# Optimization experiments

Hardware: AMD Instinct MI355X
Metric: run time of the kernel (lower is better)

Reference implementation:

```python
import jax, jax.numpy as jnp
import numpy as np

D_MODEL = 1024
NUM_HEADS = 16
HEAD_DIM = D_MODEL // NUM_HEADS


def setup_inputs() -> dict:
    key = jax.random.key(0)
    ks = jax.random.split(key, 11)
    B, S = 4, 2048
    s = 1.0 / np.sqrt(D_MODEL)
    inp = {
        "query": jax.random.normal(ks[0], (B, S, D_MODEL), jnp.float32),
        "key": jax.random.normal(ks[1], (B, S, D_MODEL), jnp.float32),
        "value": jax.random.normal(ks[2], (B, S, D_MODEL), jnp.float32),
        "Wq": jax.random.normal(ks[3], (D_MODEL, D_MODEL), jnp.float32) * s,
        "bq": jnp.zeros((D_MODEL,), jnp.float32),
        "Wk": jax.random.normal(ks[4], (D_MODEL, D_MODEL), jnp.float32) * s,
        "bk": jnp.zeros((D_MODEL,), jnp.float32),
        "Wv": jax.random.normal(ks[5], (D_MODEL, D_MODEL), jnp.float32) * s,
        "bv": jnp.zeros((D_MODEL,), jnp.float32),
        "Wo": jax.random.normal(ks[6], (D_MODEL, D_MODEL), jnp.float32) * s,
        "bo": jnp.zeros((D_MODEL,), jnp.float32),
    }
    return inp


def reference(query, key, value, Wq, bq, Wk, bk, Wv, bv, Wo, bo):
    B, S, _ = query.shape
    def proj(x, W, b):  # [B,S,D] -> [B,H,S,hd]
        y = jnp.einsum("bsd,ed->bse", x, W) + b
        return y.reshape(B, -1, NUM_HEADS, HEAD_DIM).transpose(0, 2, 1, 3)
    q = proj(query, Wq, bq)
    k = proj(key, Wk, bk)
    v = proj(value, Wv, bv)
    scores = jnp.einsum("bhqd,bhkd->bhqk", q, k) / np.sqrt(HEAD_DIM).astype(jnp.float32)
    attn = jax.nn.softmax(scores, axis=-1)
    out = jnp.einsum("bhqk,bhkd->bhqd", attn, v)
    out = out.transpose(0, 2, 1, 3).reshape(B, -1, D_MODEL)
    return jnp.einsum("bsd,ed->bse", out, Wo) + bo
```

## Files before the change

kernel.cpp:

```cpp
#include <hip/hip_runtime.h>
#include <math.h>

#define DM    1024
#define NH    16
#define HD    64
#define SEQ   2048
#define BATCH 4
#define TOKENS (BATCH * SEQ)

typedef _Float16 half2v __attribute__((ext_vector_type(2)));
typedef __fp16   fp16x2 __attribute__((ext_vector_type(2)));
typedef _Float16 half4  __attribute__((ext_vector_type(4)));
typedef _Float16 half8  __attribute__((ext_vector_type(8)));
typedef float    f32x4  __attribute__((ext_vector_type(4)));
typedef float    f32x16 __attribute__((ext_vector_type(16)));
typedef unsigned int u32x2 __attribute__((ext_vector_type(2)));
typedef unsigned int u32x4 __attribute__((ext_vector_type(4)));

typedef const __attribute__((address_space(1))) void* gas_p;
typedef __attribute__((address_space(3))) void*       las_p;

__device__ __forceinline__ void gload_lds16(const void* g, void* l) {
    __builtin_amdgcn_global_load_lds((gas_p)g, (las_p)l, 16, 0, 0);
}

__device__ __forceinline__ unsigned pack2u(float a, float b) {
    fp16x2 r = __builtin_amdgcn_cvt_pkrtz(a, b);
    return __builtin_bit_cast(unsigned, r);
}

#define MFMA16(a, b, c) __builtin_amdgcn_mfma_f32_16x16x32_f16((a), (b), (c), 0, 0, 0)
#define MFMA32(a, b, c) __builtin_amdgcn_mfma_f32_32x32x16_f16((a), (b), (c), 0, 0, 0)

__global__ __launch_bounds__(256) void cvt_all(
    const float* __restrict__ q, const float* __restrict__ k,
    const float* __restrict__ v, const float* __restrict__ wq,
    const float* __restrict__ wk, const float* __restrict__ wv,
    const float* __restrict__ wo, _Float16* __restrict__ dst)
{
    const size_t TD = (size_t)TOKENS * DM, WD = (size_t)DM * DM;
    const size_t i = ((size_t)blockIdx.x * 256 + threadIdx.x) * 4;
    const float* s; size_t off;
    if      (i <     TD)          { s = q;  off = i; }
    else if (i < 2 * TD)          { s = k;  off = i - TD; }
    else if (i < 3 * TD)          { s = v;  off = i - 2 * TD; }
    else if (i < 3 * TD + WD)     { s = wq; off = i - 3 * TD; }
    else if (i < 3 * TD + 2 * WD) { s = wk; off = i - 3 * TD - WD; }
    else if (i < 3 * TD + 3 * WD) { s = wv; off = i - 3 * TD - 2 * WD; }
    else                          { s = wo; off = i - 3 * TD - 3 * WD; }
    const float4 x = *(const float4*)(s + off);
    half4 h = { (_Float16)x.x, (_Float16)x.y, (_Float16)x.z, (_Float16)x.w };
    *(half4*)(dst + i) = h;
}

__global__ __launch_bounds__(256) void qkv_gemm(
    const _Float16* __restrict__ Abase, const _Float16* __restrict__ Wbase,
    const float* __restrict__ bq, const float* __restrict__ bk,
    const float* __restrict__ bv, _Float16* __restrict__ Cbase, float qscale)
{
    __shared__ __align__(16) _Float16 As[128 * 32];
    __shared__ __align__(16) _Float16 Ws[128 * 32];

    const int z = blockIdx.z;
    const size_t TD = (size_t)TOKENS * DM, WD = (size_t)DM * DM;
    const _Float16* A = Abase + (size_t)z * TD;
    const _Float16* W = Wbase + (size_t)z * WD;
    const float* bias = (z == 0) ? bq : (z == 1) ? bk : bv;
    _Float16* C = Cbase + (size_t)z * TD;
    const float scale = (z == 0) ? qscale : 1.0f;

    const int t = threadIdx.x;
    const int w = t >> 6, l = t & 63;
    const int tx = l & 15, quad = l >> 4;
    const int m0 = blockIdx.x * 128, n0 = blockIdx.y * 128;
    const int wm = (w & 1) * 64, wn = (w >> 1) * 64;
    const int srow = t >> 2, schk = t & 3;

    const _Float16* Ag = A + (size_t)m0 * DM;
    const _Float16* Wg = W + (size_t)n0 * DM;

    f32x4 acc[4][4] = {};

    for (int k0 = 0; k0 < DM; k0 += 32) {
        __syncthreads();
        #pragma unroll
        for (int i = 0; i < 2; ++i) {
            gload_lds16(Ag + (size_t)(i * 64 + srow) * DM + k0 + schk * 8,
                        As + (size_t)(i * 256 + (t & ~63)) * 8);
            gload_lds16(Wg + (size_t)(i * 64 + srow) * DM + k0 + schk * 8,
                        Ws + (size_t)(i * 256 + (t & ~63)) * 8);
        }
        __syncthreads();

        half8 af[4], bf[4];
        #pragma unroll
        for (int mt = 0; mt < 4; ++mt)
            af[mt] = *(const half8*)(As + (wm + mt * 16 + tx) * 32 + quad * 8);
        #pragma unroll
        for (int nt = 0; nt < 4; ++nt)
            bf[nt] = *(const half8*)(Ws + (wn + nt * 16 + tx) * 32 + quad * 8);
        #pragma unroll
        for (int mt = 0; mt < 4; ++mt)
            #pragma unroll
            for (int nt = 0; nt < 4; ++nt)
                acc[mt][nt] = MFMA16(af[mt], bf[nt], acc[mt][nt]);
    }

    float bsv[4];
    #pragma unroll
    for (int nt = 0; nt < 4; ++nt) bsv[nt] = bias[n0 + wn + nt * 16 + tx];

    #pragma unroll
    for (int mt = 0; mt < 4; ++mt) {
        #pragma unroll
        for (int nt = 0; nt < 4; ++nt) {
            const int n = n0 + wn + nt * 16 + tx;
            const int mr0 = m0 + wm + mt * 16 + quad * 4;
            const int h = n >> 6, d = n & 63;
            if (z < 2) {
                #pragma unroll
                for (int r = 0; r < 4; ++r) {
                    const int m = mr0 + r;
                    const int b = m >> 11, s = m & (SEQ - 1);
                    const float vv = (acc[mt][nt][r] + bsv[nt]) * scale;
                    C[(((size_t)b * NH + h) * SEQ + s) * HD + d] = (_Float16)vv;
                }
            } else {
                const int b = mr0 >> 11, s0 = mr0 & (SEQ - 1);
                half4 hv = { (_Float16)(acc[mt][nt][0] + bsv[nt]),
                             (_Float16)(acc[mt][nt][1] + bsv[nt]),
                             (_Float16)(acc[mt][nt][2] + bsv[nt]),
                             (_Float16)(acc[mt][nt][3] + bsv[nt]) };
                *(half4*)(C + (((size_t)b * NH + h) * HD + d) * SEQ + s0) = hv;
            }
        }
    }
}

__global__ __launch_bounds__(256) void out_gemm(
    const _Float16* __restrict__ A, const _Float16* __restrict__ W,
    const float* __restrict__ bias, float* __restrict__ C)
{
    __shared__ __align__(16) _Float16 As[128 * 32];
    __shared__ __align__(16) _Float16 Ws[128 * 32];

    const int t = threadIdx.x;
    const int w = t >> 6, l = t & 63;
    const int tx = l & 15, quad = l >> 4;
    const int m0 = blockIdx.x * 128, n0 = blockIdx.y * 128;
    const int wm = (w & 1) * 64, wn = (w >> 1) * 64;
    const int srow = t >> 2, schk = t & 3;

    const _Float16* Ag = A + (size_t)m0 * DM;
    const _Float16* Wg = W + (size_t)n0 * DM;

    f32x4 acc[4][4] = {};

    for (int k0 = 0; k0 < DM; k0 += 32) {
        __syncthreads();
        #pragma unroll
        for (int i = 0; i < 2; ++i) {
            gload_lds16(Ag + (size_t)(i * 64 + srow) * DM + k0 + schk * 8,
                        As + (size_t)(i * 256 + (t & ~63)) * 8);
            gload_lds16(Wg + (size_t)(i * 64 + srow) * DM + k0 + schk * 8,
                        Ws + (size_t)(i * 256 + (t & ~63)) * 8);
        }
        __syncthreads();

        half8 af[4], bf[4];
        #pragma unroll
        for (int mt = 0; mt < 4; ++mt)
            af[mt] = *(const half8*)(As + (wm + mt * 16 + tx) * 32 + quad * 8);
        #pragma unroll
        for (int nt = 0; nt < 4; ++nt)
            bf[nt] = *(const half8*)(Ws + (wn + nt * 16 + tx) * 32 + quad * 8);
        #pragma unroll
        for (int mt = 0; mt < 4; ++mt)
            #pragma unroll
            for (int nt = 0; nt < 4; ++nt)
                acc[mt][nt] = MFMA16(af[mt], bf[nt], acc[mt][nt]);
    }

    float bsv[4];
    #pragma unroll
    for (int nt = 0; nt < 4; ++nt) bsv[nt] = bias[n0 + wn + nt * 16 + tx];

    #pragma unroll
    for (int mt = 0; mt < 4; ++mt)
        #pragma unroll
        for (int nt = 0; nt < 4; ++nt) {
            const int n = n0 + wn + nt * 16 + tx;
            const int mr0 = m0 + wm + mt * 16 + quad * 4;
            #pragma unroll
            for (int r = 0; r < 4; ++r)
                C[(size_t)(mr0 + r) * DM + n] = acc[mt][nt][r] + bsv[nt];
        }
}

__global__ __launch_bounds__(64, 2) void flash16(
    const _Float16* __restrict__ Q, const _Float16* __restrict__ K,
    const _Float16* __restrict__ Vt, _Float16* __restrict__ AO)
{
    __shared__ __align__(16) float Ob[64 * 69];
    __shared__ float lw[64];

    const int l = threadIdx.x;
    const int lid = l & 31, hl = l >> 5;

    const int bid = blockIdx.x;
    const int xcd = bid & 7, loc = bid >> 3;
    const int bh = xcd * 8 + (loc >> 5);
    const int q0 = (loc & 31) * 64;
    const int b = bh >> 4, h = bh & 15;

    const _Float16* Qg = Q + ((size_t)bh * SEQ + q0) * HD;
    const _Float16* Kg = K + (size_t)bh * SEQ * HD;
    const _Float16* Vg = Vt + (size_t)bh * HD * SEQ;

    half8 Qf[2][4];
    #pragma unroll
    for (int qq = 0; qq < 2; ++qq)
        #pragma unroll
        for (int ks = 0; ks < 4; ++ks)
            Qf[qq][ks] = *(const half8*)(Qg + (size_t)(qq * 32 + lid) * HD + ks * 16 + hl * 8);

    f32x16 Oa[2][2] = {};
    float l2[2] = {0.f, 0.f};
    const half2v one2 = { (_Float16)1.0f, (_Float16)1.0f };

    for (int it = 0; it < SEQ / 64; ++it) {
        const int kb = it * 64;

        half8 kf[2][4];
        #pragma unroll
        for (int kt = 0; kt < 2; ++kt)
            #pragma unroll
            for (int ks = 0; ks < 4; ++ks)
                kf[kt][ks] = *(const half8*)(Kg + (size_t)(kb + kt * 32 + lid) * HD +
                                             ks * 16 + hl * 8);

        half8 vf[4][2];
        #pragma unroll
        for (int kstep = 0; kstep < 4; ++kstep)
            #pragma unroll
            for (int dt = 0; dt < 2; ++dt)
                vf[kstep][dt] = *(const half8*)(Vg + (size_t)(dt * 32 + lid) * SEQ +
                                                kb + kstep * 16 + hl * 8);

        half8 pa[2][4];
        #pragma unroll
        for (int qq = 0; qq < 2; ++qq) {
            f32x16 sacc[2];
            __builtin_amdgcn_s_setprio(1);
            #pragma unroll
            for (int kt = 0; kt < 2; ++kt) {
                f32x16 s = {};
                #pragma unroll
                for (int ks = 0; ks < 4; ++ks)
                    s = MFMA32(kf[kt][ks], Qf[qq][ks], s);
                sacc[kt] = s;
            }
            __builtin_amdgcn_s_setprio(0);

            unsigned cf[2][4][2];
            #pragma unroll
            for (int kt = 0; kt < 2; ++kt)
                #pragma unroll
                for (int g = 0; g < 4; ++g) {
                    const float p0 = __builtin_amdgcn_exp2f(sacc[kt][g * 4 + 0]);
                    const float p1 = __builtin_amdgcn_exp2f(sacc[kt][g * 4 + 1]);
                    const float p2 = __builtin_amdgcn_exp2f(sacc[kt][g * 4 + 2]);
                    const float p3 = __builtin_amdgcn_exp2f(sacc[kt][g * 4 + 3]);
                    const unsigned ca = pack2u(p0, p1);
                    const unsigned cb = pack2u(p2, p3);
                    l2[qq] = __builtin_amdgcn_fdot2(__builtin_bit_cast(half2v, ca), one2, l2[qq], false);
                    l2[qq] = __builtin_amdgcn_fdot2(__builtin_bit_cast(half2v, cb), one2, l2[qq], false);
                    cf[kt][g][0] = ca;
                    cf[kt][g][1] = cb;
                }

            #pragma unroll
            for (int kstep = 0; kstep < 4; ++kstep) {
                const int kt = kstep >> 1, g0 = (kstep & 1) * 2;
                const u32x2 r0 = __builtin_amdgcn_permlane32_swap(
                    cf[kt][g0][0], cf[kt][g0 + 1][0], false, false);
                const u32x2 r1 = __builtin_amdgcn_permlane32_swap(
                    cf[kt][g0][1], cf[kt][g0 + 1][1], false, false);
                const u32x4 pw = { r0[0], r1[0], r0[1], r1[1] };
                pa[qq][kstep] = __builtin_bit_cast(half8, pw);
            }
        }

        __builtin_amdgcn_s_setprio(1);
        #pragma unroll
        for (int kstep = 0; kstep < 4; ++kstep)
            #pragma unroll
            for (int qq = 0; qq < 2; ++qq)
                #pragma unroll
                for (int dt = 0; dt < 2; ++dt)
                    Oa[qq][dt] = MFMA32(pa[qq][kstep], vf[kstep][dt], Oa[qq][dt]);
        __builtin_amdgcn_s_setprio(0);
    }

    #pragma unroll
    for (int qq = 0; qq < 2; ++qq)
        l2[qq] += __shfl_xor(l2[qq], 32, 64);
    if (l < 32) {
        lw[l] = l2[0];
        lw[32 + l] = l2[1];
    }

    #pragma unroll
    for (int qq = 0; qq < 2; ++qq)
        #pragma unroll
        for (int dt = 0; dt < 2; ++dt)
            #pragma unroll
            for (int g = 0; g < 4; ++g)
                #pragma unroll
                for (int r = 0; r < 4; ++r)
                    Ob[(qq * 32 + g * 8 + hl * 4 + r) * 69 + dt * 32 + lid] =
                        Oa[qq][dt][g * 4 + r];
    __syncthreads();

    {
        const float inv = 1.0f / lw[l];
        _Float16* dst = AO + ((size_t)b * SEQ + q0 + l) * DM + h * HD;
        #pragma unroll
        for (int j = 0; j < 64; j += 8) {
            const f32x4 o0 = *(const f32x4*)(Ob + l * 69 + j);
            const f32x4 o1 = *(const f32x4*)(Ob + l * 69 + j + 4);
            half8 hv = { (_Float16)(o0[0] * inv), (_Float16)(o0[1] * inv),
                         (_Float16)(o0[2] * inv), (_Float16)(o0[3] * inv),
                         (_Float16)(o1[0] * inv), (_Float16)(o1[1] * inv),
                         (_Float16)(o1[2] * inv), (_Float16)(o1[3] * inv) };
            *(half8*)(dst + j) = hv;
        }
    }
}

extern "C" void kernel_launch(void* const* d_in, const int* in_sizes, int n_in,
                              void* d_out, int out_size, void* d_ws, size_t ws_size,
                              hipStream_t stream)
{
    const float* q  = (const float*)d_in[0];
    const float* k  = (const float*)d_in[1];
    const float* v  = (const float*)d_in[2];
    const float* Wq = (const float*)d_in[3];
    const float* bq = (const float*)d_in[4];
    const float* Wk = (const float*)d_in[5];
    const float* bk = (const float*)d_in[6];
    const float* Wv = (const float*)d_in[7];
    const float* bv = (const float*)d_in[8];
    const float* Wo = (const float*)d_in[9];
    const float* bo = (const float*)d_in[10];
    float* out = (float*)d_out;

    const size_t TD = (size_t)TOKENS * DM;
    const size_t WD = (size_t)DM * DM;
    _Float16* ws = (_Float16*)d_ws;
    _Float16* cvtbase = ws;
    _Float16* q16  = ws;
    _Float16* wq16 = ws + 3 * TD;
    _Float16* wo16 = wq16 + 3 * WD;
    _Float16* Qw   = ws + 3 * TD + 4 * WD;
    _Float16* Kw   = Qw + TD;
    _Float16* Vtw  = Kw + TD;
    _Float16* AOw  = Vtw + TD;

    const int gC = (int)((3 * TD + 4 * WD) / 4 / 256);
    cvt_all<<<gC, 256, 0, stream>>>(q, k, v, Wq, Wk, Wv, Wo, cvtbase);

    const float qscale = 0.18033688011112042f;
    qkv_gemm<<<dim3(TOKENS / 128, DM / 128, 3), 256, 0, stream>>>(
        q16, wq16, bq, bk, bv, Qw, qscale);

    flash16<<<dim3((SEQ / 64) * BATCH * NH), 64, 0, stream>>>(Qw, Kw, Vtw, AOw);

    out_gemm<<<dim3(TOKENS / 128, DM / 128, 1), 256, 0, stream>>>(AOw, wo16, bo, out);
}
```

Baseline: 381.6 us.

## Double-buffer K/V tiles through LDS with async global-to-LDS loads

The flash attention kernel now stages K and V tiles through swizzled, double-buffered LDS using global_load_lds, prefetching the next 32-key tile while computing the current one. Before, it loaded K and V straight from global memory into registers each iteration. The KV tile shrinks from 64 to 32 keys per iteration, and the output staging buffer now shares the same LDS pool. This is meant to hide global memory latency and cut register pressure, at the cost of more loop iterations and LDS traffic.

```diff
diff --git a/kernel.cpp b/kernel.cpp
--- a/kernel.cpp
+++ b/kernel.cpp
@@ -201,7 +201,7 @@
     const _Float16* __restrict__ Q, const _Float16* __restrict__ K,
     const _Float16* __restrict__ Vt, _Float16* __restrict__ AO)
 {
-    __shared__ __align__(16) float Ob[64 * 69];
+    __shared__ __align__(16) char pool[17664];
     __shared__ float lw[64];
 
     const int l = threadIdx.x;
@@ -217,6 +217,11 @@
     const _Float16* Kg = K + (size_t)bh * SEQ * HD;
     const _Float16* Vg = Vt + (size_t)bh * HD * SEQ;
 
+    const int srk = l >> 3;
+    const int sck = (l & 7) ^ srk;
+    const int srv = l >> 2;
+    const int scv = (l & 3) ^ ((srv >> 1) & 3);
+
     half8 Qf[2][4];
     #pragma unroll
     for (int qq = 0; qq < 2; ++qq)
@@ -228,72 +233,89 @@
     float l2[2] = {0.f, 0.f};
     const half2v one2 = { (_Float16)1.0f, (_Float16)1.0f };
 
-    for (int it = 0; it < SEQ / 64; ++it) {
-        const int kb = it * 64;
-
-        half8 kf[2][4];
-        #pragma unroll
-        for (int kt = 0; kt < 2; ++kt)
+    {
+        _Float16* KL = (_Float16*)pool;
+        _Float16* VL = (_Float16*)(pool + 8192);
+        #pragma unroll
+        for (int j = 0; j < 4; ++j) {
+            gload_lds16(Kg + (size_t)(8 * j + srk) * HD + sck * 8, KL + j * 512);
+            gload_lds16(Vg + (size_t)(16 * j + srv) * SEQ + scv * 8, VL + j * 512);
+        }
+    }
+
+    const int NIT = SEQ / 32;
+    #pragma unroll 2
+    for (int it = 0; it < NIT; ++it) {
+        if (it < NIT - 1) {
+            const int kb = (it + 1) * 32;
+            _Float16* KL = (_Float16*)(pool + ((it + 1) & 1) * 4096);
+            _Float16* VL = (_Float16*)(pool + 8192 + ((it + 1) & 1) * 4096);
+            #pragma unroll
+            for (int j = 0; j < 4; ++j) {
+                gload_lds16(Kg + (size_t)(kb + 8 * j + srk) * HD + sck * 8, KL + j * 512);
+                gload_lds16(Vg + (size_t)(16 * j + srv) * SEQ + kb + scv * 8, VL + j * 512);
+            }
+            asm volatile("s_waitcnt vmcnt(8)" ::: "memory");
+        } else {
+            asm volatile("s_waitcnt vmcnt(0)" ::: "memory");
+        }
+
+        const _Float16* KL = (const _Float16*)(pool + (it & 1) * 4096);
+        const _Float16* VL = (const _Float16*)(pool + 8192 + (it & 1) * 4096);
+
+        half8 kf[4];
+        #pragma unroll
+        for (int ks = 0; ks < 4; ++ks)
+            kf[ks] = *(const half8*)(KL + lid * 64 + (((ks * 2 + hl) ^ (lid & 7)) * 8));
+
+        half8 pa[2][2];
+        #pragma unroll
+        for (int qq = 0; qq < 2; ++qq) {
+            f32x16 s = {};
+            __builtin_amdgcn_s_setprio(1);
             #pragma unroll
             for (int ks = 0; ks < 4; ++ks)
-                kf[kt][ks] = *(const half8*)(Kg + (size_t)(kb + kt * 32 + lid) * HD +
-                                             ks * 16 + hl * 8);
-
-        half8 vf[4][2];
-        #pragma unroll
-        for (int kstep = 0; kstep < 4; ++kstep)
-            #pragma unroll
-            for (int dt = 0; dt < 2; ++dt)
-                vf[kstep][dt] = *(const half8*)(Vg + (size_t)(dt * 32 + lid) * SEQ +
-                                                kb + kstep * 16 + hl * 8);
-
-        half8 pa[2][4];
-        #pragma unroll
-        for (int qq = 0; qq < 2; ++qq) {
-            f32x16 sacc[2];
-            __builtin_amdgcn_s_setprio(1);
-            #pragma unroll
-            for (int kt = 0; kt < 2; ++kt) {
-                f32x16 s = {};
-                #pragma unroll
-                for (int ks = 0; ks < 4; ++ks)
-                    s = MFMA32(kf[kt][ks], Qf[qq][ks], s);
-                sacc[kt] = s;
+                s = MFMA32(kf[ks], Qf[qq][ks], s);
+            __builtin_amdgcn_s_setprio(0);
+
+            unsigned cf[4][2];
+            #pragma unroll
+            for (int g = 0; g < 4; ++g) {
+                const float p0 = __builtin_amdgcn_exp2f(s[g * 4 + 0]);
+                const float p1 = __builtin_amdgcn_exp2f(s[g * 4 + 1]);
+                const float p2 = __builtin_amdgcn_exp2f(s[g * 4 + 2]);
+                const float p3 = __builtin_amdgcn_exp2f(s[g * 4 + 3]);
+                const unsigned ca = pack2u(p0, p1);
+                const unsigned cb = pack2u(p2, p3);
+                l2[qq] = __builtin_amdgcn_fdot2(__builtin_bit_cast(half2v, ca), one2, l2[qq], false);
+                l2[qq] = __builtin_amdgcn_fdot2(__builtin_bit_cast(half2v, cb), one2, l2[qq], false);
+                cf[g][0] = ca;
+                cf[g][1] = cb;
             }
-            __builtin_amdgcn_s_setprio(0);
-
-            unsigned cf[2][4][2];
-            #pragma unroll
-            for (int kt = 0; kt < 2; ++kt)
-                #pragma unroll
-                for (int g = 0; g < 4; ++g) {
-                    const float p0 = __builtin_amdgcn_exp2f(sacc[kt][g * 4 + 0]);
-                    const float p1 = __builtin_amdgcn_exp2f(sacc[kt][g * 4 + 1]);
-                    const float p2 = __builtin_amdgcn_exp2f(sacc[kt][g * 4 + 2]);
-                    const float p3 = __builtin_amdgcn_exp2f(sacc[kt][g * 4 + 3]);
-                    const unsigned ca = pack2u(p0, p1);
-                    const unsigned cb = pack2u(p2, p3);
-                    l2[qq] = __builtin_amdgcn_fdot2(__builtin_bit_cast(half2v, ca), one2, l2[qq], false);
-                    l2[qq] = __builtin_amdgcn_fdot2(__builtin_bit_cast(half2v, cb), one2, l2[qq], false);
-                    cf[kt][g][0] = ca;
-                    cf[kt][g][1] = cb;
-                }
-
-            #pragma unroll
-            for (int kstep = 0; kstep < 4; ++kstep) {
-                const int kt = kstep >> 1, g0 = (kstep & 1) * 2;
+
+            #pragma unroll
+            for (int kstep = 0; kstep < 2; ++kstep) {
+                const int g0 = kstep * 2;
                 const u32x2 r0 = __builtin_amdgcn_permlane32_swap(
-                    cf[kt][g0][0], cf[kt][g0 + 1][0], false, false);
+                    cf[g0][0], cf[g0 + 1][0], false, false);
                 const u32x2 r1 = __builtin_amdgcn_permlane32_swap(
-                    cf[kt][g0][1], cf[kt][g0 + 1][1], false, false);
+                    cf[g0][1], cf[g0 + 1][1], false, false);
                 const u32x4 pw = { r0[0], r1[0], r0[1], r1[1] };
                 pa[qq][kstep] = __builtin_bit_cast(half8, pw);
             }
         }
 
+        half8 vf[2][2];
+        #pragma unroll
+        for (int kstep = 0; kstep < 2; ++kstep)
+            #pragma unroll
+            for (int dt = 0; dt < 2; ++dt)
+                vf[kstep][dt] = *(const half8*)(VL + (dt * 32 + lid) * 32 +
+                                                (((kstep * 2 + hl) ^ ((lid >> 1) & 3)) * 8));
+
         __builtin_amdgcn_s_setprio(1);
         #pragma unroll
-        for (int kstep = 0; kstep < 4; ++kstep)
+        for (int kstep = 0; kstep < 2; ++kstep)
             #pragma unroll
             for (int qq = 0; qq < 2; ++qq)
                 #pragma unroll
@@ -310,6 +332,7 @@
         lw[32 + l] = l2[1];
     }
 
+    float* Ob = (float*)pool;
     #pragma unroll
     for (int qq = 0; qq < 2; ++qq)
         #pragma unroll
```

Measured after the change: 369.8 us. 3.1% less time.
